# Optimization experiments

Measured on AMD Instinct MI355X. Metric: run time of the kernel, lower is better.

Reference implementation:

```python
import jax, jax.numpy as jnp
import numpy as np

L, B, E = 2048, 4, 512      # seq len (= MoE group dim), batch (= MoE tokens-per-group), embed
H = 8                        # attention heads
FF = 2048                    # expert hidden dim
NE = 5                       # num experts
EPS = 1e-9
THRESHOLD = 0.2              # second_threshold_eval
CAP_FACTOR = 2.0             # capacity_factor_eval
MIN_CAP = 4
CAP = max(min(B, int(B * 2 * CAP_FACTOR / NE)), MIN_CAP)  # expert capacity per group


def setup_inputs() -> dict:
    key = jax.random.key(0)
    ks = jax.random.split(key, 8)
    s = lambda k, shape, scale: jax.random.normal(k, shape, jnp.float32) * scale
    return {
        "x": s(ks[0], (L, B, E), 1.0),
        "ln1_w": jnp.ones((E,), jnp.float32), "ln1_b": jnp.zeros((E,), jnp.float32),
        "ln2_w": jnp.ones((E,), jnp.float32), "ln2_b": jnp.zeros((E,), jnp.float32),
        "in_proj_w": s(ks[1], (3 * E, E), E ** -0.5), "in_proj_b": jnp.zeros((3 * E,), jnp.float32),
        "out_proj_w": s(ks[2], (E, E), E ** -0.5), "out_proj_b": jnp.zeros((E,), jnp.float32),
        "w_gating": s(ks[3], (E, NE), E ** -0.5),
        "w1": s(ks[4], (NE, E, FF), E ** -0.5),
        "w2": s(ks[5], (NE, FF, E), FF ** -0.5),
    }


def layer_norm(x, w, b, eps=1e-5):
    mu = x.mean(-1, keepdims=True)
    var = ((x - mu) ** 2).mean(-1, keepdims=True)
    return (x - mu) * jax.lax.rsqrt(var + eps) * w + b


def mha(x, wi, bi, wo, bo):
    # x: (L, B, E) as in torch nn.MultiheadAttention (batch_first=False)
    qkv = x @ wi.T + bi
    q, k, v = jnp.split(qkv, 3, axis=-1)
    hd = E // H
    q = q.reshape(L, B, H, hd) * (hd ** -0.5)
    k = k.reshape(L, B, H, hd)
    v = v.reshape(L, B, H, hd)
    scores = jnp.einsum('lbhd,mbhd->bhlm', q, k)          # (B,H,L,L)
    attn = jax.nn.softmax(scores, axis=-1)
    out = jnp.einsum('bhlm,mbhd->lbhd', attn, v).reshape(L, B, E)
    return out @ wo.T + bo


def top2_gating(x, w_gating, key):
    # x: (b=L, n=B, d); gshard-style top-2 gating, eval mode, 'random' second policy
    raw = jax.nn.softmax(x @ w_gating, axis=-1)            # (b,n,e)
    f32 = raw.dtype
    idx1 = jnp.argmax(raw, -1)
    gate1 = jnp.take_along_axis(raw, idx1[..., None], -1)[..., 0]
    m1 = jax.nn.one_hot(idx1, NE, dtype=f32)
    raw2 = raw * (1.0 - m1)
    idx2 = jnp.argmax(raw2, -1)
    gate2 = jnp.take_along_axis(raw2, idx2[..., None], -1)[..., 0]
    m2 = jax.nn.one_hot(idx2, NE, dtype=f32)
    denom = gate1 + gate2 + EPS
    gate1, gate2 = gate1 / denom, gate2 / denom
    # second_policy == 'random': keep second expert with prob gate2/threshold
    probs = jax.random.uniform(key, gate2.shape, f32)
    m2 = m2 * (probs < gate2 / THRESHOLD).astype(f32)[..., None]
    # capacity bookkeeping (exclusive cumsum over tokens, dim=-2)
    pos1 = (jnp.cumsum(m1, axis=-2) - m1) * m1
    m1 = m1 * (pos1 < CAP).astype(f32)
    m1_count = m1.sum(-2, keepdims=True)
    m1_flat = m1.sum(-1)
    pos1 = pos1.sum(-1)
    gate1 = gate1 * m1_flat
    pos2 = ((jnp.cumsum(m2, axis=-2) - m2) + m1_count) * m2
    m2 = m2 * (pos2 < CAP).astype(f32)
    m2_flat = m2.sum(-1)
    pos2 = pos2.sum(-1)
    gate2 = gate2 * m2_flat
    ohc = lambda p: jax.nn.one_hot(p.astype(jnp.int32), CAP, dtype=f32)  # safe: OOB -> zeros
    combine = (gate1[..., None, None] * m1_flat[..., None, None]
               * jax.nn.one_hot(idx1, NE, dtype=f32)[..., None] * ohc(pos1)[..., None, :]
               + gate2[..., None, None] * m2_flat[..., None, None]
               * jax.nn.one_hot(idx2, NE, dtype=f32)[..., None] * ohc(pos2)[..., None, :])
    dispatch = (combine != 0).astype(f32)
    return dispatch, combine


def moe(x, w_gating, w1, w2, key):
    dispatch, combine = top2_gating(x, w_gating, key)       # (b,n,e,c)
    ein = jnp.einsum('bnd,bnec->ebcd', x, dispatch)         # gather to experts
    h = jax.nn.relu(jnp.einsum('ebcd,edh->ebch', ein, w1))
    eo = jnp.einsum('ebch,ehd->ebcd', h, w2)
    return jnp.einsum('bnec,ebcd->bnd', combine, eo)        # scatter back


def reference(x, ln1_w, ln1_b, ln2_w, ln2_b, in_proj_w, in_proj_b,
              out_proj_w, out_proj_b, w_gating, w1, w2):
    key = jax.random.key(42)  # fixed RNG for 'random' second policy (eval determinism)
    h = layer_norm(x, ln1_w, ln1_b)
    x = x + mha(h, in_proj_w, in_proj_b, out_proj_w, out_proj_b)
    h2 = layer_norm(x, ln2_w, ln2_b)
    x = x + moe(h2, w_gating, w1, w2, key)
    return x
```

## Files before the change

kernel.cpp:

```cpp
#include <hip/hip_runtime.h>

#define DI __device__ __forceinline__

namespace {

constexpr int kL  = 2048;
constexpr int kB  = 4;
constexpr int kE  = 512;
constexpr int kHD = 64;
constexpr int kFF = 2048;
constexpr int kNE = 5;
constexpr int kT  = 8192;
constexpr int kCAP = 4;

using bf16x8 = __attribute__((ext_vector_type(8))) short;
using f32x4  = __attribute__((ext_vector_type(4))) float;

DI float bf2f(unsigned short u) { return __uint_as_float(((unsigned)u) << 16); }
DI unsigned short f2bf(float f) {
  unsigned u = __float_as_uint(f);
  u = u + 0x7FFFu + ((u >> 16) & 1u);
  return (unsigned short)(u >> 16);
}

DI unsigned rotl(unsigned v, int d) { return (v << d) | (v >> (32 - d)); }

DI void threefry(unsigned& x0, unsigned& x1) {
  const unsigned K1 = 0u, K2 = 42u, K3 = 0x1BD11BDAu ^ 0u ^ 42u;
  x0 += K1; x1 += K2;
  x0 += x1; x1 = rotl(x1, 13); x1 ^= x0;
  x0 += x1; x1 = rotl(x1, 15); x1 ^= x0;
  x0 += x1; x1 = rotl(x1, 26); x1 ^= x0;
  x0 += x1; x1 = rotl(x1,  6); x1 ^= x0;
  x0 += K2; x1 += K3 + 1u;
  x0 += x1; x1 = rotl(x1, 17); x1 ^= x0;
  x0 += x1; x1 = rotl(x1, 29); x1 ^= x0;
  x0 += x1; x1 = rotl(x1, 16); x1 ^= x0;
  x0 += x1; x1 = rotl(x1, 24); x1 ^= x0;
  x0 += K3; x1 += K1 + 2u;
  x0 += x1; x1 = rotl(x1, 13); x1 ^= x0;
  x0 += x1; x1 = rotl(x1, 15); x1 ^= x0;
  x0 += x1; x1 = rotl(x1, 26); x1 ^= x0;
  x0 += x1; x1 = rotl(x1,  6); x1 ^= x0;
  x0 += K1; x1 += K2 + 3u;
  x0 += x1; x1 = rotl(x1, 17); x1 ^= x0;
  x0 += x1; x1 = rotl(x1, 29); x1 ^= x0;
  x0 += x1; x1 = rotl(x1, 16); x1 ^= x0;
  x0 += x1; x1 = rotl(x1, 24); x1 ^= x0;
  x0 += K2; x1 += K3 + 4u;
  x0 += x1; x1 = rotl(x1, 13); x1 ^= x0;
  x0 += x1; x1 = rotl(x1, 15); x1 ^= x0;
  x0 += x1; x1 = rotl(x1, 26); x1 ^= x0;
  x0 += x1; x1 = rotl(x1,  6); x1 ^= x0;
  x0 += K3; x1 += K1 + 5u;
}

__global__ __launch_bounds__(256) void f2bf_kernel(
    const float* __restrict__ src, unsigned short* __restrict__ dst, int n4) {
  int i = blockIdx.x * blockDim.x + threadIdx.x;
  if (i >= n4) return;
  float4 v = ((const float4*)src)[i];
  ushort4 u;
  u.x = f2bf(v.x); u.y = f2bf(v.y); u.z = f2bf(v.z); u.w = f2bf(v.w);
  ((ushort4*)dst)[i] = u;
}

__global__ __launch_bounds__(256) void wsplit_kernel(
    const float* __restrict__ src, unsigned short* __restrict__ hi,
    unsigned short* __restrict__ lo, int n4) {
  int i = blockIdx.x * blockDim.x + threadIdx.x;
  if (i >= n4) return;
  float4 v = ((const float4*)src)[i];
  float va[4] = {v.x, v.y, v.z, v.w};
  ushort4 h4, l4;
  unsigned short* hp = (unsigned short*)&h4;
  unsigned short* lp = (unsigned short*)&l4;
  #pragma unroll
  for (int j = 0; j < 4; ++j) {
    unsigned short h = f2bf(va[j]);
    hp[j] = h;
    lp[j] = f2bf(va[j] - bf2f(h));
  }
  ((ushort4*)hi)[i] = h4;
  ((ushort4*)lo)[i] = l4;
}

template <int SPLIT>
__global__ __launch_bounds__(256) void ln_kernel(
    const float* __restrict__ x, const float* __restrict__ w,
    const float* __restrict__ b, float* __restrict__ out,
    unsigned short* __restrict__ ohi, unsigned short* __restrict__ olo) {
  int row = blockIdx.x;
  const float* xr = x + (size_t)row * kE;
  int t = threadIdx.x;
  float2 v = *(const float2*)(xr + t * 2);
  __shared__ float red[4];
  float s = v.x + v.y;
  #pragma unroll
  for (int m = 32; m; m >>= 1) s += __shfl_xor(s, m);
  if ((t & 63) == 0) red[t >> 6] = s;
  __syncthreads();
  float mu = (red[0] + red[1] + red[2] + red[3]) * (1.0f / kE);
  float dx = v.x - mu, dy = v.y - mu;
  float q = dx * dx + dy * dy;
  #pragma unroll
  for (int m = 32; m; m >>= 1) q += __shfl_xor(q, m);
  __syncthreads();
  if ((t & 63) == 0) red[t >> 6] = q;
  __syncthreads();
  float var = (red[0] + red[1] + red[2] + red[3]) * (1.0f / kE);
  float inv = 1.0f / sqrtf(var + 1e-5f);
  float ox = dx * inv * w[t * 2]     + b[t * 2];
  float oy = dy * inv * w[t * 2 + 1] + b[t * 2 + 1];
  if (SPLIT) {
    size_t base = (size_t)row * kE + t * 2;
    unsigned short hx = f2bf(ox), hy = f2bf(oy);
    ohi[base] = hx; ohi[base + 1] = hy;
    olo[base] = f2bf(ox - bf2f(hx)); olo[base + 1] = f2bf(oy - bf2f(hy));
  } else {
    *(float2*)(out + (size_t)row * kE + t * 2) = make_float2(ox, oy);
  }
}

template <int RES, int SPLITOUT>
__global__ __launch_bounds__(256) void dsgemm_kernel(
    const unsigned short* __restrict__ Ahi, const unsigned short* __restrict__ Alo,
    const unsigned short* __restrict__ Bhi, const unsigned short* __restrict__ Blo,
    const float* __restrict__ biasp, const float* __restrict__ Rp,
    float* __restrict__ Cf, unsigned short* __restrict__ Chi,
    unsigned short* __restrict__ Clo, int M, int N, int K) {
  __shared__ unsigned short AHs[128][40];
  __shared__ unsigned short ALs[128][40];
  __shared__ unsigned short BHs[128][40];
  __shared__ unsigned short BLs[128][40];

  int nwg = gridDim.x * gridDim.y;
  int bid = blockIdx.y * gridDim.x + blockIdx.x;
  int swz = (bid & 7) * (nwg >> 3) + (bid >> 3);
  int wx = swz % gridDim.x, wy = swz / gridDim.x;
  const int m0 = wy * 128;
  const int n0 = wx * 128;

  const int t = threadIdx.x;
  const int lane = t & 63, w = t >> 6;
  const int wm = w >> 1, wn = w & 1;
  const int ar = t >> 1, ah = t & 1;

  f32x4 acc[4][4];
  #pragma unroll
  for (int i = 0; i < 4; ++i)
    #pragma unroll
    for (int j = 0; j < 4; ++j)
      acc[i][j] = (f32x4){0.f, 0.f, 0.f, 0.f};

  uint4 aH[2], aL[2], bH[2], bL[2];
  auto gload = [&](int k0) {
    size_t aoff = (size_t)(m0 + ar) * K + k0 + ah * 16;
    aH[0] = *(const uint4*)(Ahi + aoff); aH[1] = *(const uint4*)(Ahi + aoff + 8);
    aL[0] = *(const uint4*)(Alo + aoff); aL[1] = *(const uint4*)(Alo + aoff + 8);
    size_t boff = (size_t)(n0 + ar) * K + k0 + ah * 16;
    bH[0] = *(const uint4*)(Bhi + boff); bH[1] = *(const uint4*)(Bhi + boff + 8);
    bL[0] = *(const uint4*)(Blo + boff); bL[1] = *(const uint4*)(Blo + boff + 8);
  };
  gload(0);

  const int kg = (lane >> 4) * 8;
  const int mr = lane & 15;

  for (int k0 = 0; k0 < K; k0 += 32) {
    __syncthreads();
    *(uint4*)&AHs[ar][ah * 16]     = aH[0];
    *(uint4*)&AHs[ar][ah * 16 + 8] = aH[1];
    *(uint4*)&ALs[ar][ah * 16]     = aL[0];
    *(uint4*)&ALs[ar][ah * 16 + 8] = aL[1];
    *(uint4*)&BHs[ar][ah * 16]     = bH[0];
    *(uint4*)&BHs[ar][ah * 16 + 8] = bH[1];
    *(uint4*)&BLs[ar][ah * 16]     = bL[0];
    *(uint4*)&BLs[ar][ah * 16 + 8] = bL[1];
    __syncthreads();
    if (k0 + 32 < K) gload(k0 + 32);

    bf16x8 afH[4], afL[4], bfH[4], bfL[4];
    #pragma unroll
    for (int i = 0; i < 4; ++i) {
      afH[i] = *(const bf16x8*)&AHs[wm * 64 + i * 16 + mr][kg];
      afL[i] = *(const bf16x8*)&ALs[wm * 64 + i * 16 + mr][kg];
    }
    #pragma unroll
    for (int j = 0; j < 4; ++j) {
      bfH[j] = *(const bf16x8*)&BHs[wn * 64 + j * 16 + mr][kg];
      bfL[j] = *(const bf16x8*)&BLs[wn * 64 + j * 16 + mr][kg];
    }
    #pragma unroll
    for (int i = 0; i < 4; ++i)
      #pragma unroll
      for (int j = 0; j < 4; ++j) {
        acc[i][j] = __builtin_amdgcn_mfma_f32_16x16x32_bf16(afH[i], bfH[j], acc[i][j], 0, 0, 0);
        acc[i][j] = __builtin_amdgcn_mfma_f32_16x16x32_bf16(afH[i], bfL[j], acc[i][j], 0, 0, 0);
        acc[i][j] = __builtin_amdgcn_mfma_f32_16x16x32_bf16(afL[i], bfH[j], acc[i][j], 0, 0, 0);
      }
  }

  const int lr4 = (lane >> 4) * 4;
  const int lc = lane & 15;
  #pragma unroll
  for (int i = 0; i < 4; ++i)
    #pragma unroll
    for (int r = 0; r < 4; ++r) {
      int row = m0 + wm * 64 + i * 16 + lr4 + r;
      size_t crow = (size_t)row * N;
      #pragma unroll
      for (int j = 0; j < 4; ++j) {
        int col = n0 + wn * 64 + j * 16 + lc;
        float v = acc[i][j][r] + biasp[col];
        if (RES) v += Rp[crow + col];
        if (SPLITOUT) {
          unsigned short hi = f2bf(v);
          Chi[crow + col] = hi;
          Clo[crow + col] = f2bf(v - bf2f(hi));
        } else {
          Cf[crow + col] = v;
        }
      }
    }
}

template <int GATHER, int RELU, int K, int N>
__global__ __launch_bounds__(256) void moe_mfma_kernel(
    const unsigned short* __restrict__ Abf, const unsigned short* __restrict__ Bbf,
    unsigned short* __restrict__ Cbf,
    const int* __restrict__ gatherp, const int* __restrict__ cntp,
    const int* __restrict__ basep) {
  __shared__ unsigned short As[128][40];
  __shared__ unsigned short Bs[128][40];

  const int e = blockIdx.z;
  const int M = cntp[e];
  const int rowOff = basep[e];
  if ((int)blockIdx.y * 128 >= M) return;
  const unsigned short* Bg = Bbf + (size_t)e * K * N;
  const int m0 = blockIdx.y * 128;
  const int n0 = blockIdx.x * 128;
  const int t = threadIdx.x;
  const int lane = t & 63, w = t >> 6;
  const int wm = w >> 1, wn = w & 1;

  const int ar = t >> 1, ah = t & 1;
  size_t abase;
  {
    int r = m0 + ar;
    int mm = M - 1; r = r < mm ? r : mm;
    if (GATHER) r = gatherp[rowOff + r];
    else        r += rowOff;
    abase = (size_t)r * K;
  }
  const int bk = t >> 3, bn = (t & 7) * 16;

  f32x4 acc[4][4];
  #pragma unroll
  for (int i = 0; i < 4; ++i)
    #pragma unroll
    for (int j = 0; j < 4; ++j)
      acc[i][j] = (f32x4){0.f, 0.f, 0.f, 0.f};

  uint4 aR0, aR1, bR0, bR1;
  auto gload = [&](int k0) {
    aR0 = *(const uint4*)(Abf + abase + k0 + ah * 16);
    aR1 = *(const uint4*)(Abf + abase + k0 + ah * 16 + 8);
    bR0 = *(const uint4*)(Bg + (size_t)(k0 + bk) * N + n0 + bn);
    bR1 = *(const uint4*)(Bg + (size_t)(k0 + bk) * N + n0 + bn + 8);
  };
  gload(0);

  const int kg = (lane >> 4) * 8;
  const int mr = lane & 15;

  for (int k0 = 0; k0 < K; k0 += 32) {
    __syncthreads();
    *(uint4*)&As[ar][ah * 16]     = aR0;
    *(uint4*)&As[ar][ah * 16 + 8] = aR1;
    {
      unsigned short tmp[16];
      *(uint4*)tmp       = bR0;
      *(uint4*)(tmp + 8) = bR1;
      #pragma unroll
      for (int j = 0; j < 16; ++j) Bs[bn + j][bk] = tmp[j];
    }
    __syncthreads();
    if (k0 + 32 < K) gload(k0 + 32);

    bf16x8 af[4], bfr[4];
    #pragma unroll
    for (int i = 0; i < 4; ++i)
      af[i] = *(const bf16x8*)&As[wm * 64 + i * 16 + mr][kg];
    #pragma unroll
    for (int j = 0; j < 4; ++j)
      bfr[j] = *(const bf16x8*)&Bs[wn * 64 + j * 16 + mr][kg];
    #pragma unroll
    for (int i = 0; i < 4; ++i)
      #pragma unroll
      for (int j = 0; j < 4; ++j)
        acc[i][j] = __builtin_amdgcn_mfma_f32_16x16x32_bf16(
            af[i], bfr[j], acc[i][j], 0, 0, 0);
  }

  const int lr4 = (lane >> 4) * 4;
  const int lc = lane & 15;
  #pragma unroll
  for (int i = 0; i < 4; ++i)
    #pragma unroll
    for (int r = 0; r < 4; ++r) {
      int row = m0 + wm * 64 + i * 16 + lr4 + r;
      if (row >= M) continue;
      size_t crow = (size_t)(row + rowOff) * N;
      #pragma unroll
      for (int j = 0; j < 4; ++j) {
        float v = acc[i][j][r];
        if (RELU) v = v > 0.f ? v : 0.f;
        Cbf[crow + n0 + wn * 64 + j * 16 + lc] = f2bf(v);
      }
    }
}

DI int pswz(int row) { return ((row >> 1) & 7) << 3; }

__global__ __launch_bounds__(256) void flash_kernel(
    const unsigned short* __restrict__ qh, const unsigned short* __restrict__ ql,
    unsigned short* __restrict__ aohi, unsigned short* __restrict__ aolo) {
  __shared__ unsigned short KPhi[64][72];
  __shared__ unsigned short KPlo[64][72];
  __shared__ unsigned short Vthi[64][72];
  __shared__ unsigned short Vtlo[64][72];

  int bid = blockIdx.y * 32 + blockIdx.x;
  int swzb = (bid & 7) * 128 + (bid >> 3);
  const int bh = swzb >> 5;
  const int qt = swzb & 31;
  const int b = bh >> 3, h = bh & 7;
  const int t = threadIdx.x;
  const int w = t >> 6, lane = t & 63;
  const int l15 = lane & 15, l4 = lane >> 4;
  const int lr = t >> 2;
  const int dbase = (t & 3) * 16;
  const int vd = t & 63;
  const int kv0 = (t >> 6) * 16;

  bf16x8 qhi[2], qlo[2];
  {
    int qglob = qt * 64 + w * 16 + l15;
    size_t qoff = ((size_t)(qglob * kB + b)) * (3 * kE) + h * kHD;
    #pragma unroll
    for (int ks = 0; ks < 2; ++ks) {
      qhi[ks] = *(const bf16x8*)(qh + qoff + ks * 32 + l4 * 8);
      qlo[ks] = *(const bf16x8*)(ql + qoff + ks * 32 + l4 * 8);
    }
  }

  float m_i[4], l_i[4];
  f32x4 Oacc[4];
  #pragma unroll
  for (int r = 0; r < 4; ++r) { m_i[r] = -1e30f; l_i[r] = 0.f; }
  #pragma unroll
  for (int df = 0; df < 4; ++df) Oacc[df] = (f32x4){0.f, 0.f, 0.f, 0.f};

  uint4 kh[2], kl[2];
  unsigned short vh[16], vl[16];
  auto kv_load = [&](int ktile) {
    size_t koff = ((size_t)((ktile * 64 + lr) * kB + b)) * (3 * kE) + kE + h * kHD + dbase;
    kh[0] = *(const uint4*)(qh + koff);
    kh[1] = *(const uint4*)(qh + koff + 8);
    kl[0] = *(const uint4*)(ql + koff);
    kl[1] = *(const uint4*)(ql + koff + 8);
    #pragma unroll
    for (int j = 0; j < 16; ++j) {
      size_t voff = ((size_t)((ktile * 64 + kv0 + j) * kB + b)) * (3 * kE) + 2 * kE + h * kHD + vd;
      vh[j] = qh[voff];
      vl[j] = ql[voff];
    }
  };
  kv_load(0);

  for (int kt = 0; kt < 32; ++kt) {
    __syncthreads();
    {
      int sw = pswz(lr);
      *(uint4*)&KPhi[lr][(dbase)     ^ sw] = kh[0];
      *(uint4*)&KPhi[lr][(dbase + 8) ^ sw] = kh[1];
      *(uint4*)&KPlo[lr][(dbase)     ^ sw] = kl[0];
      *(uint4*)&KPlo[lr][(dbase + 8) ^ sw] = kl[1];
      int swv = pswz(vd);
      *(uint4*)&Vthi[vd][(kv0)     ^ swv] = ((uint4*)vh)[0];
      *(uint4*)&Vthi[vd][(kv0 + 8) ^ swv] = ((uint4*)vh)[1];
      *(uint4*)&Vtlo[vd][(kv0)     ^ swv] = ((uint4*)vl)[0];
      *(uint4*)&Vtlo[vd][(kv0 + 8) ^ swv] = ((uint4*)vl)[1];
    }
    __syncthreads();
    if (kt + 1 < 32) kv_load(kt + 1);

    f32x4 acc[4];
    #pragma unroll
    for (int nf = 0; nf < 4; ++nf) acc[nf] = (f32x4){0.f, 0.f, 0.f, 0.f};
    #pragma unroll
    for (int ks = 0; ks < 2; ++ks) {
      #pragma unroll
      for (int nf = 0; nf < 4; ++nf) {
        int krow = nf * 16 + l15;
        int off = (ks * 32 + l4 * 8) ^ pswz(krow);
        bf16x8 kkh = *(const bf16x8*)&KPhi[krow][off];
        bf16x8 kkl = *(const bf16x8*)&KPlo[krow][off];
        acc[nf] = __builtin_amdgcn_mfma_f32_16x16x32_bf16(qhi[ks], kkh, acc[nf], 0, 0, 0);
        acc[nf] = __builtin_amdgcn_mfma_f32_16x16x32_bf16(qhi[ks], kkl, acc[nf], 0, 0, 0);
        acc[nf] = __builtin_amdgcn_mfma_f32_16x16x32_bf16(qlo[ks], kkh, acc[nf], 0, 0, 0);
      }
    }
    #pragma unroll
    for (int nf = 0; nf < 4; ++nf)
      #pragma unroll
      for (int r = 0; r < 4; ++r) acc[nf][r] *= 0.125f;

    float pv[4][4];
    float alpha[4];
    #pragma unroll
    for (int r = 0; r < 4; ++r) {
      float tm = fmaxf(fmaxf(acc[0][r], acc[1][r]), fmaxf(acc[2][r], acc[3][r]));
      #pragma unroll
      for (int m = 1; m < 16; m <<= 1) tm = fmaxf(tm, __shfl_xor(tm, m));
      float mn = fmaxf(m_i[r], tm);
      alpha[r] = __expf(m_i[r] - mn);
      m_i[r] = mn;
      float rs = 0.f;
      #pragma unroll
      for (int nf = 0; nf < 4; ++nf) {
        float p = __expf(acc[nf][r] - mn);
        pv[r][nf] = p;
        rs += p;
      }
      #pragma unroll
      for (int m = 1; m < 16; m <<= 1) rs += __shfl_xor(rs, m);
      l_i[r] = l_i[r] * alpha[r] + rs;
    }
    #pragma unroll
    for (int df = 0; df < 4; ++df)
      #pragma unroll
      for (int r = 0; r < 4; ++r) Oacc[df][r] *= alpha[r];

    __syncthreads();
    #pragma unroll
    for (int r = 0; r < 4; ++r) {
      int qrow = w * 16 + l4 * 4 + r;
      int sw = pswz(qrow);
      #pragma unroll
      for (int nf = 0; nf < 4; ++nf) {
        int scol = (nf * 16 + l15) ^ sw;
        float p = pv[r][nf];
        unsigned short hi = f2bf(p);
        KPhi[qrow][scol] = hi;
        KPlo[qrow][scol] = f2bf(p - bf2f(hi));
      }
    }
    __syncthreads();

    {
      int prow = w * 16 + l15;
      int swp = pswz(prow);
      #pragma unroll
      for (int ks = 0; ks < 2; ++ks) {
        int koff = ks * 32 + l4 * 8;
        bf16x8 ph = *(const bf16x8*)&KPhi[prow][koff ^ swp];
        bf16x8 pl = *(const bf16x8*)&KPlo[prow][koff ^ swp];
        #pragma unroll
        for (int df = 0; df < 4; ++df) {
          int vrow = df * 16 + l15;
          int off = koff ^ pswz(vrow);
          bf16x8 vvh = *(const bf16x8*)&Vthi[vrow][off];
          bf16x8 vvl = *(const bf16x8*)&Vtlo[vrow][off];
          Oacc[df] = __builtin_amdgcn_mfma_f32_16x16x32_bf16(ph, vvh, Oacc[df], 0, 0, 0);
          Oacc[df] = __builtin_amdgcn_mfma_f32_16x16x32_bf16(ph, vvl, Oacc[df], 0, 0, 0);
          Oacc[df] = __builtin_amdgcn_mfma_f32_16x16x32_bf16(pl, vvh, Oacc[df], 0, 0, 0);
        }
      }
    }
  }

  #pragma unroll
  for (int r = 0; r < 4; ++r) {
    float inv = 1.0f / l_i[r];
    int l = qt * 64 + w * 16 + l4 * 4 + r;
    size_t obase = ((size_t)(l * kB + b)) * kE + h * kHD;
    #pragma unroll
    for (int df = 0; df < 4; ++df) {
      float o = Oacc[df][r] * inv;
      unsigned short hi = f2bf(o);
      aohi[obase + df * 16 + l15] = hi;
      aolo[obase + df * 16 + l15] = f2bf(o - bf2f(hi));
    }
  }
}

__global__ __launch_bounds__(256) void gating_kernel(
    const float* __restrict__ h2, const float* __restrict__ wg,
    int* __restrict__ e1, int* __restrict__ e2,
    float* __restrict__ g1, float* __restrict__ g2,
    int* __restrict__ keepr) {
  __shared__ float swg[kE * kNE];
  for (int i = threadIdx.x; i < kE * kNE; i += 256) swg[i] = wg[i];
  __syncthreads();
  int w = threadIdx.x >> 6, lane = threadIdx.x & 63;
  int tok = blockIdx.x * 4 + w;
  const float* xr = h2 + (size_t)tok * kE;
  float a0=0,a1=0,a2=0,a3=0,a4=0;
  for (int d = lane; d < kE; d += 64) {
    float xv = xr[d];
    a0 = fmaf(xv, swg[d*5+0], a0);
    a1 = fmaf(xv, swg[d*5+1], a1);
    a2 = fmaf(xv, swg[d*5+2], a2);
    a3 = fmaf(xv, swg[d*5+3], a3);
    a4 = fmaf(xv, swg[d*5+4], a4);
  }
  #pragma unroll
  for (int m = 32; m; m >>= 1) {
    a0 += __shfl_xor(a0, m); a1 += __shfl_xor(a1, m); a2 += __shfl_xor(a2, m);
    a3 += __shfl_xor(a3, m); a4 += __shfl_xor(a4, m);
  }
  if (lane == 0) {
    float lg[5] = {a0, a1, a2, a3, a4};
    float mx = lg[0];
    #pragma unroll
    for (int e = 1; e < 5; ++e) mx = fmaxf(mx, lg[e]);
    float ex[5], ssum = 0.f;
    #pragma unroll
    for (int e = 0; e < 5; ++e) { ex[e] = expf(lg[e] - mx); ssum += ex[e]; }
    float raw[5];
    #pragma unroll
    for (int e = 0; e < 5; ++e) raw[e] = ex[e] / ssum;
    int i1 = 0; float v1 = raw[0];
    #pragma unroll
    for (int e = 1; e < 5; ++e) if (raw[e] > v1) { v1 = raw[e]; i1 = e; }
    int i2 = 0; float v2 = -1.f;
    #pragma unroll
    for (int e = 0; e < 5; ++e) if (e != i1 && raw[e] > v2) { v2 = raw[e]; i2 = e; }
    float denom = v1 + v2 + 1e-9f;
    float G1 = v1 / denom, G2 = v2 / denom;
    unsigned x0 = 0u, x1 = (unsigned)tok;
    threefry(x0, x1);
    unsigned bits = x0 ^ x1;
    float u = __uint_as_float((bits >> 9) | 0x3F800000u) - 1.0f;
    int kr = (u < G2 / 0.2f) ? 1 : 0;
    e1[tok] = i1; e2[tok] = i2; g1[tok] = G1; g2[tok] = G2; keepr[tok] = kr;
  }
}

__global__ __launch_bounds__(256) void plan_kernel(
    const int* __restrict__ e1, const int* __restrict__ e2,
    const int* __restrict__ keepr,
    int* __restrict__ slot1, int* __restrict__ slot2, int* __restrict__ tot) {
  int l = blockIdx.x * blockDim.x + threadIdx.x;
  if (l >= kL) return;
  int base = l * 4;
  int e1v[4], e2v[4], kr[4];
  #pragma unroll
  for (int n = 0; n < 4; ++n) {
    e1v[n] = e1[base + n]; e2v[n] = e2[base + n]; kr[n] = keepr[base + n];
  }
  int c1[5] = {0,0,0,0,0};
  int s1[4];
  #pragma unroll
  for (int n = 0; n < 4; ++n) {
    int e = e1v[n];
    int p = 0;
    #pragma unroll
    for (int q = 0; q < 5; ++q) if (q == e) p = c1[q];
    s1[n] = p;
    #pragma unroll
    for (int q = 0; q < 5; ++q) c1[q] += (q == e);
  }
  int run[5] = {0,0,0,0,0};
  int s2[4];
  #pragma unroll
  for (int n = 0; n < 4; ++n) {
    s2[n] = -1;
    if (kr[n]) {
      int e = e2v[n];
      int p = 0;
      #pragma unroll
      for (int q = 0; q < 5; ++q) if (q == e) p = c1[q] + run[q];
      if (p < kCAP) s2[n] = p;
      #pragma unroll
      for (int q = 0; q < 5; ++q) run[q] += (q == e);
    }
  }
  #pragma unroll
  for (int n = 0; n < 4; ++n) { slot1[base + n] = s1[n]; slot2[base + n] = s2[n]; }
  int adm[5] = {0,0,0,0,0};
  #pragma unroll
  for (int n = 0; n < 4; ++n)
    if (s2[n] >= 0) {
      #pragma unroll
      for (int q = 0; q < 5; ++q) adm[q] += (q == e2v[n]);
    }
  #pragma unroll
  for (int q = 0; q < 5; ++q) tot[l * kNE + q] = c1[q] + adm[q];
}

__global__ __launch_bounds__(256) void scan_kernel(
    const int* __restrict__ tot, int* __restrict__ gbase, int* __restrict__ cnt) {
  int e = blockIdx.x;
  int t = threadIdx.x;
  int lane = t & 63, w = t >> 6;
  __shared__ int wsum[4];
  __shared__ int carry;
  if (t == 0) carry = 0;
  __syncthreads();
  for (int chunk = 0; chunk < kL / 256; ++chunk) {
    int g = chunk * 256 + t;
    int v = tot[g * kNE + e];
    int inc = v;
    #pragma unroll
    for (int off = 1; off < 64; off <<= 1) {
      int u = __shfl_up(inc, off);
      if (lane >= off) inc += u;
    }
    if (lane == 63) wsum[w] = inc;
    __syncthreads();
    int wb = 0;
    #pragma unroll
    for (int i = 0; i < 4; ++i) wb += (i < w) ? wsum[i] : 0;
    int total = wsum[0] + wsum[1] + wsum[2] + wsum[3];
    gbase[g * kNE + e] = carry + wb + inc - v;
    __syncthreads();
    if (t == 0) carry += total;
    __syncthreads();
  }
  if (t == 0) cnt[e] = carry;
}

__global__ void bases_kernel(const int* __restrict__ cnt, int* __restrict__ base) {
  if (threadIdx.x == 0 && blockIdx.x == 0) {
    int a = 0;
    #pragma unroll
    for (int e = 0; e < kNE; ++e) { base[e] = a; a += cnt[e]; }
  }
}

__global__ __launch_bounds__(256) void rowmap_kernel(
    const int* __restrict__ e1, const int* __restrict__ e2,
    const int* __restrict__ slot1, const int* __restrict__ slot2,
    const int* __restrict__ gbase, const int* __restrict__ ebase,
    int* __restrict__ rowOf1, int* __restrict__ rowOf2,
    int* __restrict__ tokOfRow) {
  int tok = blockIdx.x * blockDim.x + threadIdx.x;
  if (tok >= kT) return;
  int l = tok >> 2;
  int a = e1[tok];
  int r1 = ebase[a] + gbase[l * kNE + a] + slot1[tok];
  rowOf1[tok] = r1;
  tokOfRow[r1] = tok;
  int s2 = slot2[tok];
  int r2 = -1;
  if (s2 >= 0) {
    int bq = e2[tok];
    r2 = ebase[bq] + gbase[l * kNE + bq] + s2;
    tokOfRow[r2] = tok;
  }
  rowOf2[tok] = r2;
}

__global__ __launch_bounds__(128) void combine_kernel(
    const float* __restrict__ xres, const unsigned short* __restrict__ eo,
    const float* __restrict__ g1, const float* __restrict__ g2,
    const int* __restrict__ rowOf1, const int* __restrict__ rowOf2,
    float* __restrict__ out) {
  int tok = blockIdx.x;
  int t = threadIdx.x;
  float4 o = *(const float4*)(xres + (size_t)tok * kE + t * 4);
  int p1 = rowOf1[tok];
  float G1 = g1[tok];
  ushort4 a = *(const ushort4*)(eo + (size_t)p1 * kE + t * 4);
  o.x += G1 * bf2f(a.x); o.y += G1 * bf2f(a.y);
  o.z += G1 * bf2f(a.z); o.w += G1 * bf2f(a.w);
  int p2 = rowOf2[tok];
  if (p2 >= 0) {
    float G2 = g2[tok];
    ushort4 c = *(const ushort4*)(eo + (size_t)p2 * kE + t * 4);
    o.x += G2 * bf2f(c.x); o.y += G2 * bf2f(c.y);
    o.z += G2 * bf2f(c.z); o.w += G2 * bf2f(c.w);
  }
  *(float4*)(out + (size_t)tok * kE + t * 4) = o;
}

}

extern "C" void kernel_launch(void* const* d_in, const int* in_sizes, int n_in,
                              void* d_out, int out_size, void* d_ws, size_t ws_size,
                              hipStream_t stream) {
  (void)in_sizes; (void)n_in; (void)out_size;
  const float* x    = (const float*)d_in[0];
  const float* ln1w = (const float*)d_in[1];
  const float* ln1b = (const float*)d_in[2];
  const float* ln2w = (const float*)d_in[3];
  const float* ln2b = (const float*)d_in[4];
  const float* wqkv = (const float*)d_in[5];
  const float* bqkv = (const float*)d_in[6];
  const float* wo   = (const float*)d_in[7];
  const float* bo   = (const float*)d_in[8];
  const float* wg   = (const float*)d_in[9];
  const float* w1   = (const float*)d_in[10];
  const float* w2   = (const float*)d_in[11];
  float* out = (float*)d_out;

  if (ws_size < (size_t)134742016) return;
  float* ws   = (float*)d_ws;
  float* xres = ws;
  unsigned short* w1bf   = (unsigned short*)(ws + 4194304);
  unsigned short* w2bf   = (unsigned short*)(ws + 6815744);
  unsigned short* wqkvhi = (unsigned short*)(ws + 9437184);
  unsigned short* wqkvlo = (unsigned short*)(ws + 9830400);
  unsigned short* wohi   = (unsigned short*)(ws + 10223616);
  unsigned short* wolo   = (unsigned short*)(ws + 10354688);
  int* ibuf = (int*)(ws + 10485760);
  unsigned short* h1hi  = (unsigned short*)(ws + 10616832);
  unsigned short* h1lo  = (unsigned short*)(ws + 12713984);
  unsigned short* qkvhi = (unsigned short*)(ws + 14811136);
  unsigned short* qkvlo = (unsigned short*)(ws + 21102592);
  unsigned short* aohi  = (unsigned short*)(ws + 27394048);
  unsigned short* aolo  = (unsigned short*)(ws + 29491200);
  float* h2             = ws + 10616832;
  unsigned short* eobf  = (unsigned short*)(ws + 10616832);
  unsigned short* h2bf  = (unsigned short*)(ws + 14811136);
  unsigned short* hmoe  = (unsigned short*)(ws + 16908288);

  int* e1      = ibuf;
  int* e2      = e1 + kT;
  float* g1f   = (float*)(e2 + kT);
  float* g2f   = g1f + kT;
  int* keepr   = (int*)(g2f + kT);
  int* slot1   = keepr + kT;
  int* slot2   = slot1 + kT;
  int* rowOf1  = slot2 + kT;
  int* rowOf2  = rowOf1 + kT;
  int* tot     = rowOf2 + kT;
  int* gbase   = tot + kL * kNE;
  int* tokOfRow= gbase + kL * kNE;
  int* cnt     = tokOfRow + 2 * kT;
  int* ebase   = cnt + 8;

  f2bf_kernel<<<5120, 256, 0, stream>>>(w1, w1bf, kNE * kE * kFF / 4);
  f2bf_kernel<<<5120, 256, 0, stream>>>(w2, w2bf, kNE * kFF * kE / 4);
  wsplit_kernel<<<768, 256, 0, stream>>>(wqkv, wqkvhi, wqkvlo, 1536 * kE / 4);
  wsplit_kernel<<<256, 256, 0, stream>>>(wo, wohi, wolo, kE * kE / 4);
  ln_kernel<1><<<kT, 256, 0, stream>>>(x, ln1w, ln1b, nullptr, h1hi, h1lo);
  dsgemm_kernel<0,1><<<dim3(12, 64), 256, 0, stream>>>(
      h1hi, h1lo, wqkvhi, wqkvlo, bqkv, nullptr,
      nullptr, qkvhi, qkvlo, kT, 1536, kE);
  flash_kernel<<<dim3(32, 32, 1), 256, 0, stream>>>(qkvhi, qkvlo, aohi, aolo);
  dsgemm_kernel<1,0><<<dim3(4, 64), 256, 0, stream>>>(
      aohi, aolo, wohi, wolo, bo, x,
      xres, nullptr, nullptr, kT, kE, kE);
  ln_kernel<0><<<kT, 256, 0, stream>>>(xres, ln2w, ln2b, h2, nullptr, nullptr);
  gating_kernel<<<kL, 256, 0, stream>>>(h2, wg, e1, e2, g1f, g2f, keepr);
  f2bf_kernel<<<4096, 256, 0, stream>>>(h2, h2bf, kT * kE / 4);
  plan_kernel<<<kL / 256, 256, 0, stream>>>(e1, e2, keepr, slot1, slot2, tot);
  scan_kernel<<<kNE, 256, 0, stream>>>(tot, gbase, cnt);
  bases_kernel<<<1, 32, 0, stream>>>(cnt, ebase);
  rowmap_kernel<<<kT / 256, 256, 0, stream>>>(
      e1, e2, slot1, slot2, gbase, ebase, rowOf1, rowOf2, tokOfRow);
  moe_mfma_kernel<1,1,kE,kFF><<<dim3(16, 64, kNE), 256, 0, stream>>>(
      h2bf, w1bf, hmoe, tokOfRow, cnt, ebase);
  moe_mfma_kernel<0,0,kFF,kE><<<dim3(4, 64, kNE), 256, 0, stream>>>(
      hmoe, w2bf, eobf, nullptr, cnt, ebase);
  combine_kernel<<<kT, 128, 0, stream>>>(
      xres, eobf, g1f, g2f, rowOf1, rowOf2, out);
}
```

Measured before the change: 719.3 us.

## Pre-transpose expert weights to N-major bf16 and fuse LN2 bf16 output

Expert weight conversion now also transposes w1/w2 into N-major bf16 layout through a shared-memory tile. The MoE GEMM can then load B tiles with contiguous vector stores into LDS instead of a 16-way scalar transposed scatter. Separately, LayerNorm-2 now writes the bf16 copy of its output directly, which removes the standalone f2bf pass over h2. The cost is a transpose kernel with strided LDS reads in place of a plain elementwise conversion.

```diff
diff --git a/kernel.cpp b/kernel.cpp
--- a/kernel.cpp
+++ b/kernel.cpp
@@ -55,14 +55,31 @@
   x0 += K3; x1 += K1 + 5u;
 }
 
-__global__ __launch_bounds__(256) void f2bf_kernel(
-    const float* __restrict__ src, unsigned short* __restrict__ dst, int n4) {
-  int i = blockIdx.x * blockDim.x + threadIdx.x;
-  if (i >= n4) return;
-  float4 v = ((const float4*)src)[i];
-  ushort4 u;
-  u.x = f2bf(v.x); u.y = f2bf(v.y); u.z = f2bf(v.z); u.w = f2bf(v.w);
-  ((ushort4*)dst)[i] = u;
+__global__ __launch_bounds__(256) void tsplit_kernel(
+    const float* __restrict__ in, unsigned short* __restrict__ outbf,
+    int R, int C) {
+  __shared__ unsigned short tile[64][72];
+  int z = blockIdx.z;
+  int c0 = blockIdx.x * 64, r0 = blockIdx.y * 64;
+  int t = threadIdx.x;
+  int rr = t >> 2, cb = (t & 3) * 16;
+  const float* src = in + ((size_t)z * R + r0 + rr) * C + c0 + cb;
+  #pragma unroll
+  for (int j = 0; j < 4; ++j) {
+    float4 v = *(const float4*)(src + 4 * j);
+    tile[rr][cb + 4*j + 0] = f2bf(v.x);
+    tile[rr][cb + 4*j + 1] = f2bf(v.y);
+    tile[rr][cb + 4*j + 2] = f2bf(v.z);
+    tile[rr][cb + 4*j + 3] = f2bf(v.w);
+  }
+  __syncthreads();
+  int cc = t >> 2, rb = (t & 3) * 16;
+  unsigned short tmp[16];
+  #pragma unroll
+  for (int j = 0; j < 16; ++j) tmp[j] = tile[rb + j][cc];
+  unsigned short* dst = outbf + ((size_t)z * C + c0 + cc) * R + r0 + rb;
+  *(uint4*)(dst)     = ((uint4*)tmp)[0];
+  *(uint4*)(dst + 8) = ((uint4*)tmp)[1];
 }
 
 __global__ __launch_bounds__(256) void wsplit_kernel(
@@ -112,13 +129,16 @@
   float inv = 1.0f / sqrtf(var + 1e-5f);
   float ox = dx * inv * w[t * 2]     + b[t * 2];
   float oy = dy * inv * w[t * 2 + 1] + b[t * 2 + 1];
-  if (SPLIT) {
-    size_t base = (size_t)row * kE + t * 2;
+  size_t base = (size_t)row * kE + t * 2;
+  if (SPLIT == 1) {
     unsigned short hx = f2bf(ox), hy = f2bf(oy);
     ohi[base] = hx; ohi[base + 1] = hy;
     olo[base] = f2bf(ox - bf2f(hx)); olo[base + 1] = f2bf(oy - bf2f(hy));
+  } else if (SPLIT == 2) {
+    *(float2*)(out + base) = make_float2(ox, oy);
+    ohi[base] = f2bf(ox); ohi[base + 1] = f2bf(oy);
   } else {
-    *(float2*)(out + (size_t)row * kE + t * 2) = make_float2(ox, oy);
+    *(float2*)(out + base) = make_float2(ox, oy);
   }
 }
 
@@ -254,7 +274,7 @@
     else        r += rowOff;
     abase = (size_t)r * K;
   }
-  const int bk = t >> 3, bn = (t & 7) * 16;
+  size_t bbase = (size_t)(n0 + ar) * K;
 
   f32x4 acc[4][4];
   #pragma unroll
@@ -267,8 +287,8 @@
   auto gload = [&](int k0) {
     aR0 = *(const uint4*)(Abf + abase + k0 + ah * 16);
     aR1 = *(const uint4*)(Abf + abase + k0 + ah * 16 + 8);
-    bR0 = *(const uint4*)(Bg + (size_t)(k0 + bk) * N + n0 + bn);
-    bR1 = *(const uint4*)(Bg + (size_t)(k0 + bk) * N + n0 + bn + 8);
+    bR0 = *(const uint4*)(Bg + bbase + k0 + ah * 16);
+    bR1 = *(const uint4*)(Bg + bbase + k0 + ah * 16 + 8);
   };
   gload(0);
 
@@ -279,13 +299,8 @@
     __syncthreads();
     *(uint4*)&As[ar][ah * 16]     = aR0;
     *(uint4*)&As[ar][ah * 16 + 8] = aR1;
-    {
-      unsigned short tmp[16];
-      *(uint4*)tmp       = bR0;
-      *(uint4*)(tmp + 8) = bR1;
-      #pragma unroll
-      for (int j = 0; j < 16; ++j) Bs[bn + j][bk] = tmp[j];
-    }
+    *(uint4*)&Bs[ar][ah * 16]     = bR0;
+    *(uint4*)&Bs[ar][ah * 16 + 8] = bR1;
     __syncthreads();
     if (k0 + 32 < K) gload(k0 + 32);
 
@@ -711,8 +726,8 @@
   if (ws_size < (size_t)134742016) return;
   float* ws   = (float*)d_ws;
   float* xres = ws;
-  unsigned short* w1bf   = (unsigned short*)(ws + 4194304);
-  unsigned short* w2bf   = (unsigned short*)(ws + 6815744);
+  unsigned short* w1t    = (unsigned short*)(ws + 4194304);
+  unsigned short* w2t    = (unsigned short*)(ws + 6815744);
   unsigned short* wqkvhi = (unsigned short*)(ws + 9437184);
   unsigned short* wqkvlo = (unsigned short*)(ws + 9830400);
   unsigned short* wohi   = (unsigned short*)(ws + 10223616);
@@ -744,8 +759,8 @@
   int* cnt     = tokOfRow + 2 * kT;
   int* ebase   = cnt + 8;
 
-  f2bf_kernel<<<5120, 256, 0, stream>>>(w1, w1bf, kNE * kE * kFF / 4);
-  f2bf_kernel<<<5120, 256, 0, stream>>>(w2, w2bf, kNE * kFF * kE / 4);
+  tsplit_kernel<<<dim3(32, 8, kNE), 256, 0, stream>>>(w1, w1t, kE, kFF);
+  tsplit_kernel<<<dim3(8, 32, kNE), 256, 0, stream>>>(w2, w2t, kFF, kE);
   wsplit_kernel<<<768, 256, 0, stream>>>(wqkv, wqkvhi, wqkvlo, 1536 * kE / 4);
   wsplit_kernel<<<256, 256, 0, stream>>>(wo, wohi, wolo, kE * kE / 4);
   ln_kernel<1><<<kT, 256, 0, stream>>>(x, ln1w, ln1b, nullptr, h1hi, h1lo);
@@ -756,18 +771,17 @@
   dsgemm_kernel<1,0><<<dim3(4, 64), 256, 0, stream>>>(
       aohi, aolo, wohi, wolo, bo, x,
       xres, nullptr, nullptr, kT, kE, kE);
-  ln_kernel<0><<<kT, 256, 0, stream>>>(xres, ln2w, ln2b, h2, nullptr, nullptr);
+  ln_kernel<2><<<kT, 256, 0, stream>>>(xres, ln2w, ln2b, h2, h2bf, nullptr);
   gating_kernel<<<kL, 256, 0, stream>>>(h2, wg, e1, e2, g1f, g2f, keepr);
-  f2bf_kernel<<<4096, 256, 0, stream>>>(h2, h2bf, kT * kE / 4);
   plan_kernel<<<kL / 256, 256, 0, stream>>>(e1, e2, keepr, slot1, slot2, tot);
   scan_kernel<<<kNE, 256, 0, stream>>>(tot, gbase, cnt);
   bases_kernel<<<1, 32, 0, stream>>>(cnt, ebase);
   rowmap_kernel<<<kT / 256, 256, 0, stream>>>(
       e1, e2, slot1, slot2, gbase, ebase, rowOf1, rowOf2, tokOfRow);
   moe_mfma_kernel<1,1,kE,kFF><<<dim3(16, 64, kNE), 256, 0, stream>>>(
-      h2bf, w1bf, hmoe, tokOfRow, cnt, ebase);
+      h2bf, w1t, hmoe, tokOfRow, cnt, ebase);
   moe_mfma_kernel<0,0,kFF,kE><<<dim3(4, 64, kNE), 256, 0, stream>>>(
-      hmoe, w2bf, eobf, nullptr, cnt, ebase);
+      hmoe, w2t, eobf, nullptr, cnt, ebase);
   combine_kernel<<<kT, 128, 0, stream>>>(
       xres, eobf, g1f, g2f, rowOf1, rowOf2, out);
 }
```

After: 614.4 us. 14.6% less time.
